# Optimization experiments

Hardware: AMD Instinct MI355X
Metric: run time of the kernel (lower is better)

Reference implementation:

```python
import jax, jax.numpy as jnp
import numpy as np
from jax import lax

N = 200; E = 3200; HID = 64; NH = 16; OUT = 2 * HID; CAT = NH * OUT  # CAT = 2048
ALPHA = 0.2


def _gat(h, e_attr, adj, n2n, W, a_s, a_d, a_e, We, concat):
    # edge-feature-aware GAT head: logits from Wh_i, Wh_j and projected node2node feats
    Nn = h.shape[0]
    Wh = h @ W                                       # [N, out]
    ee = ((n2n @ We) @ a_e).reshape(Nn, Nn)          # [N, N] edge-feature term
    logits = jax.nn.leaky_relu((Wh @ a_s)[:, None] + (Wh @ a_d)[None, :] + ee,
                               negative_slope=ALPHA)
    logits = jnp.where(adj > 0, logits, -1e9)        # mask to graph structure
    att = jax.nn.softmax(logits, axis=1)
    h2 = att @ Wh
    if concat:
        h2 = jax.nn.elu(h2)
    return h2, jax.nn.elu(e_attr @ We)               # updated node + edge features


def _edge_pool(x, eidx, e, w, b):
    # static-shape edge pooling: score edges, gate nodes by mean incident score
    src, dst = eidx[0], eidx[1]
    s = jax.nn.sigmoid(jnp.concatenate([x[src], x[dst], e], axis=1) @ w + b)  # [E]
    deg = jax.ops.segment_sum(jnp.ones_like(s), src, num_segments=x.shape[0])
    ns = jax.ops.segment_sum(s, src, num_segments=x.shape[0]) / (deg + 1e-6)
    return x * ns[:, None], e * s[:, None]


def _gpool(x, w, b):
    # GlobalAttention: gate_nn = Linear+Sigmoid, softmax over nodes, weighted sum
    gate = jax.nn.softmax(jax.nn.sigmoid(x @ w + b), axis=0)  # [N, 1]
    return jnp.sum(gate * x, axis=0, keepdims=True)           # [1, D]


def _adj_n2n(Nn, eidx, eattr):
    # vectorized version of the per-edge Python loop in _get_adj_node2node
    src, dst = eidx[0], eidx[1]
    adj = jnp.zeros((Nn, Nn), eattr.dtype).at[src, dst].set(1.0)
    n2n = jnp.zeros((Nn * Nn, eattr.shape[1]), eattr.dtype).at[src * Nn + dst].set(eattr)
    return adj, n2n


def _lstm_dir(x, Wih, Whh, b):
    # one LSTM direction over seq x [T, Din] (PyTorch i,f,g,o gate order)
    Hh = Whh.shape[1]
    def step(carry, xt):
        h, c = carry
        g = xt @ Wih.T + h @ Whh.T + b
        i, f, gg, o = jnp.split(g, 4)
        c = jax.nn.sigmoid(f) * c + jax.nn.sigmoid(i) * jnp.tanh(gg)
        h = jax.nn.sigmoid(o) * jnp.tanh(c)
        return (h, c), h
    (_, _), ys = lax.scan(step, (jnp.zeros(Hh, x.dtype), jnp.zeros(Hh, x.dtype)), x)
    return ys


def setup_inputs():
    key = jax.random.key(0)
    ks = iter(jax.random.split(key, 64))
    def rn(shape, scale=0.05):
        return jax.random.normal(next(ks), shape, jnp.float32) * scale
    inp = {}
    for g in (1, 2):
        eidx = jax.random.randint(next(ks), (2, E), 0, N)
        eattr = rn((E, HID), 1.0)
        adj, n2n = _adj_n2n(N, eidx, eattr)
        inp['features%d' % g] = rn((N, HID), 1.0)
        inp['edge_index%d' % g] = eidx
        inp['edgesAttr%d' % g] = eattr
        inp['adjacency%d' % g] = adj
        inp['node2node%d' % g] = n2n
    inp.update(dict(
        W_h=rn((HID, HID)),
        W_gat=rn((NH, HID, OUT)), a_src=rn((NH, OUT)), a_dst=rn((NH, OUT)),
        a_e=rn((NH, OUT)), We_gat=rn((NH, HID, OUT)),
        W_out=rn((CAT, OUT)), ao_src=rn((OUT,)), ao_dst=rn((OUT,)), ao_e=rn((OUT,)),
        We_out=rn((CAT, OUT)),
        ep1_w=rn((3 * CAT,)), ep1_b=rn(()),
        ep2_w=rn((3 * OUT,)), ep2_b=rn(()),
        g1_w=rn((HID, 1)), g1_b=rn((1,)),
        g2_w=rn((CAT, 1)), g2_b=rn((1,)),
        g3_w=rn((OUT, 1)), g3_b=rn((1,)),
        Wih0=rn((2, 512, 35 * HID)), Whh0=rn((2, 512, 128)), b0=rn((2, 512)),
        Wih1=rn((2, 512, 256)), Whh1=rn((2, 512, 128)), b1=rn((2, 512)),
        fc_w=rn((256, 2)), fc_b=rn((2,)),
    ))
    return inp


def reference(features1, features2, edge_index1, edge_index2, edgesAttr1, edgesAttr2,
              adjacency1, adjacency2, node2node1, node2node2,
              W_h, W_gat, a_src, a_dst, a_e, We_gat,
              W_out, ao_src, ao_dst, ao_e, We_out,
              ep1_w, ep1_b, ep2_w, ep2_b,
              g1_w, g1_b, g2_w, g2_b, g3_w, g3_b,
              Wih0, Whh0, b0, Wih1, Whh1, b1, fc_w, fc_b):
    def graph(feat, eidx, eattr, adj, n2n):
        h = jax.nn.elu(feat @ W_h)                              # SingleNodeAttentionLayer
        hs = [_gpool(h, g1_w, g1_b)]
        outs = [_gat(h, eattr, adj, n2n, W_gat[i], a_src[i], a_dst[i], a_e[i],
                     We_gat[i], True) for i in range(NH)]
        h = jnp.concatenate([o[0] for o in outs], axis=1)       # [N, 2048]
        eattr = jnp.concatenate([o[1] for o in outs], axis=1)   # [E, 2048]
        h, eattr = _edge_pool(h, eidx, eattr, ep1_w, ep1_b)
        hs.append(_gpool(h, g2_w, g2_b))
        adj2, n2n2 = _adj_n2n(h.shape[0], eidx, eattr)          # dense [N*N, 2048]
        h, eattr = _gat(h, eattr, adj2, n2n2, W_out, ao_src, ao_dst, ao_e, We_out, False)
        h, eattr = _edge_pool(h, eidx, eattr, ep2_w, ep2_b)
        hs.append(_gpool(h, g3_w, g3_b))
        return jnp.concatenate(hs, axis=1)                      # [1, 35*HID]

    h1 = graph(features1, edge_index1, edgesAttr1, adjacency1, node2node1)
    h2 = graph(features2, edge_index2, edgesAttr2, adjacency2, node2node2)
    x = jnp.concatenate([h1, h2], axis=0)                       # seq [2, 2240]
    for Wih, Whh, b in ((Wih0, Whh0, b0), (Wih1, Whh1, b1)):
        f = _lstm_dir(x, Wih[0], Whh[0], b[0])
        r = _lstm_dir(x[::-1], Wih[1], Whh[1], b[1])[::-1]
        x = jnp.concatenate([f, r], axis=1)                     # [2, 256]
    logits = x[-1] @ fc_w + fc_b
    return jax.nn.softmax(logits)[None, :]                      # [1, nclass]
```

## Files before the change

### kernel.cpp

```cpp
#include <hip/hip_runtime.h>
#include <math.h>

#define DI static __device__ __forceinline__

DI float eluf(float x){ return x > 0.f ? x : expm1f(x); }
DI float lreluf(float x){ return x > 0.f ? x : 0.2f*x; }
DI float sigmf(float x){ return 1.f/(1.f+expf(-x)); }

typedef unsigned short u16;
typedef unsigned int   u32;
typedef __attribute__((ext_vector_type(8))) short short8_t;
typedef __attribute__((ext_vector_type(4))) float f32x4;

DI u16 bf16rne(float f){
  u32 u = __float_as_uint(f);
  u += 0x7fffu + ((u>>16)&1u);
  return (u16)(u>>16);
}

DI f32x4 bmfma(short8_t a, short8_t b, f32x4 c){
  return __builtin_amdgcn_mfma_f32_16x16x32_bf16(a, b, c, 0, 0, 0);
}

constexpr int N=200, E=3200, HID=64, NH=16, OUTD=128, CAT=2048, SEQD=2240;

constexpr int OH0   = 0;
constexpr int OWH   = OH0 + N*HID;
constexpr int OASN  = OWH + NH*N*OUTD;
constexpr int OADN  = OASN + NH*N;
constexpr int OH1   = OADN + NH*N;
constexpr int OXW1  = OH1 + N*CAT;
constexpr int OXW2  = OXW1 + 256;
constexpr int OEW1  = OXW2 + 256;
constexpr int OS1   = OEW1 + E;
constexpr int ODEG1 = OS1 + E;
constexpr int OSS1  = ODEG1 + 256;
constexpr int ORAW1 = OSS1 + 256;
constexpr int OWH2  = ORAW1 + 256;
constexpr int OAS2  = OWH2 + N*OUTD;
constexpr int OAD2  = OAS2 + 256;
constexpr int OEWV  = OAD2 + 256;
constexpr int OH2B  = OEWV + E;
constexpr int OXS2  = OH2B + N*OUTD;
constexpr int OXD2  = OXS2 + 256;
constexpr int ODEG2 = OXD2 + 256;
constexpr int OSS2  = ODEG2 + 256;
constexpr int ORAW2 = OSS2 + 256;
constexpr int ORAW3 = ORAW2 + 256;
constexpr int PGF   = ORAW3 + 256;
constexpr int GLOBF = 10624;
constexpr int TOTF  = GLOBF + 2*PGF;

__device__ __attribute__((aligned(16))) float G_F[TOTF];
__device__ float G_E2PART[(size_t)4*2*E*OUTD];
__device__ float G_EDOTH[2*NH*E];
__device__ float G_WHHT[2*2*128*512];
__device__ int   G_PIDX[2*N*N];
__device__ __attribute__((aligned(16))) u16 G_WGAT_T[NH*OUTD*HID];
__device__ __attribute__((aligned(16))) u16 G_WOUT_T[OUTD*CAT];
__device__ __attribute__((aligned(16))) u16 G_EATTR_BF[2*E*HID];

DI float* gf(int g){ return G_F + GLOBF + (size_t)g*PGF; }
DI float* gwe_ae(){ return G_F; }
DI float* gv_e(){ return G_F + 1024; }
DI float* gy0(){ return G_F + 3072; }
DI float* gy1(){ return G_F + 3584; }
DI float* gxseq(){ return G_F + 4096; }
DI float* gxg(){ return G_F + 8576; }
DI int*   gpidx(int g){ return G_PIDX + g*N*N; }

struct GraphIn {
  const float *feat, *eattr, *adj, *n2n;
  const int   *eidx;
};

struct Params {
  GraphIn g[2];
  const float *W_h, *W_gat, *a_src, *a_dst, *a_e, *We_gat;
  const float *W_out, *ao_src, *ao_dst, *ao_e, *We_out;
  const float *ep1_w, *ep1_b, *ep2_w, *ep2_b;
  const float *g1_w, *g1_b, *g2_w, *g2_b, *g3_w, *g3_b;
  const float *Wih0, *Whh0, *b0, *Wih1, *Whh1, *b1, *fc_w, *fc_b;
  float *out;
};

constexpr int ZPG  = 2*E + 1024 + 768;
constexpr int IB_Z = (2*ZPG+255)/256;
constexpr int IB_C = (2*N*N+255)/256;
constexpr int IB_D = (2*2*512*128)/256;
constexpr int IB_E = (NH*HID+CAT+3)/4;
constexpr int IB_H = (2*N+3)/4;
constexpr int IB_W1 = (NH*OUTD*HID)/256;
constexpr int IB_W2 = (OUTD*CAT)/256;
constexpr int IB_EA = (2*E*HID)/256;
__global__ void k_init(Params P){
  int b = blockIdx.x, tid = threadIdx.x;
  if (b < IB_Z){
    int i = b*256 + tid;
    if (i < 2*ZPG){
      int g = i/ZPG, r = i%ZPG;
      int addr;
      if (r < E) addr = OEW1+r;
      else if (r < 2*E) addr = OEWV+(r-E);
      else if (r < 2*E+512) addr = ODEG1+(r-2*E);
      else if (r < 2*E+1024) addr = ODEG2+(r-2*E-512);
      else if (r < 2*E+1280) addr = OXW1+(r-2*E-1024);
      else if (r < 2*E+1536) addr = OXW2+(r-2*E-1280);
      else addr = ORAW2+(r-2*E-1536);
      gf(g)[addr] = 0.f;
    }
  } else if (b < IB_Z+IB_C){
    int i = (b-IB_Z)*256 + tid; if (i < 2*N*N) G_PIDX[i] = -1;
  } else if (b < IB_Z+IB_C+IB_D){
    int idx = (b-IB_Z-IB_C)*256 + tid;
    int l = idx >> 17;
    int r = idx & 131071;
    int d = r >> 16;
    int r2 = r & 65535;
    int gate = r2 & 511;
    int k = r2 >> 9;
    const float* Whh = l ? P.Whh1 : P.Whh0;
    G_WHHT[idx] = Whh[((size_t)d*512+gate)*128 + k];
  } else if (b < IB_Z+IB_C+IB_D+IB_E){
    int gid = (b-IB_Z-IB_C-IB_D)*4 + (tid>>6);
    int lane = tid & 63;
    if (gid < NH*HID){
      int h = gid/HID, c = gid%HID;
      const float* W = P.We_gat + (size_t)(h*HID+c)*OUTD;
      const float* a = P.a_e + h*OUTD;
      float acc = 0.f;
      for (int o=lane;o<OUTD;o+=64) acc += W[o]*a[o];
      for (int off=32;off>0;off>>=1) acc += __shfl_down(acc,off);
      if (lane==0) gwe_ae()[gid] = acc;
    } else if (gid < NH*HID+CAT){
      int c = gid - NH*HID;
      const float* W = P.We_out + (size_t)c*OUTD;
      float acc = 0.f;
      for (int o=lane;o<OUTD;o+=64) acc += W[o]*P.ao_e[o];
      for (int off=32;off>0;off>>=1) acc += __shfl_down(acc,off);
      if (lane==0) gv_e()[c] = acc;
    }
  } else if (b < IB_Z+IB_C+IB_D+IB_E+IB_H){
    int unit = (b-IB_Z-IB_C-IB_D-IB_E)*4 + (tid>>6);
    if (unit >= 2*N) return;
    int g = unit / N, n = unit % N, c = tid & 63;
    const float* feat = P.g[g].feat;
    float acc = 0.f;
    for (int k=0;k<HID;k++) acc += feat[n*HID+k]*P.W_h[k*HID+c];
    float v = eluf(acc);
    float* f = gf(g);
    f[OH0 + n*HID + c] = v;
    float r = v*P.g1_w[c];
    for (int off=32;off>0;off>>=1) r += __shfl_down(r,off);
    if (c==0) f[ORAW1+n] = r;
  } else if (b < IB_Z+IB_C+IB_D+IB_E+IB_H+IB_W1){
    int i = (b-(IB_Z+IB_C+IB_D+IB_E+IB_H))*256 + tid;
    int h = i>>13, o = (i>>6)&127, c = i&63;
    G_WGAT_T[i] = bf16rne(P.We_gat[(size_t)(h*HID+c)*OUTD + o]);
  } else if (b < IB_Z+IB_C+IB_D+IB_E+IB_H+IB_W1+IB_W2){
    int i = (b-(IB_Z+IB_C+IB_D+IB_E+IB_H+IB_W1))*256 + tid;
    int n = i>>11, q = i&2047;
    G_WOUT_T[i] = bf16rne(P.We_out[(size_t)q*OUTD + n]);
  } else {
    int i = (b-(IB_Z+IB_C+IB_D+IB_E+IB_H+IB_W1+IB_W2))*256 + tid;
    int g = i >= E*HID ? 1 : 0;
    G_EATTR_BF[i] = bf16rne(P.g[g].eattr[i - g*E*HID]);
  }
}
constexpr int IB_TOT = IB_Z+IB_C+IB_D+IB_E+IB_H+IB_W1+IB_W2+IB_EA;


DI void e2p_body(Params& P, int idx, char* smem){
  int g = idx/400, r2 = idx%400, hg = r2/100, eb = r2%100;
  int tid = threadIdx.x;
  int wave = tid>>6, lane = tid&63, l16 = lane&15, l4 = lane>>4;
  u16* Tlds = (u16*)smem;
  int e0 = eb*32;
  int nt0 = wave*2;
  const u16* ea = G_EATTR_BF + ((size_t)g*E + e0)*HID;
  short8_t af00 = *(const short8_t*)(ea + l16*HID + l4*8);
  short8_t af01 = *(const short8_t*)(ea + l16*HID + 32 + l4*8);
  short8_t af10 = *(const short8_t*)(ea + (16+l16)*HID + l4*8);
  short8_t af11 = *(const short8_t*)(ea + (16+l16)*HID + 32 + l4*8);
  float ew1p0[4] = {0.f,0.f,0.f,0.f}, ewvp0[4] = {0.f,0.f,0.f,0.f};
  float ew1p1[4] = {0.f,0.f,0.f,0.f}, ewvp1[4] = {0.f,0.f,0.f,0.f};
  for (int hh=0; hh<4; hh++){
    int h = hg*4 + hh;
    const u16* Wg = G_WGAT_T + (size_t)h*OUTD*HID;
    #pragma unroll
    for (int nn=0; nn<2; nn++){
      int nt = nt0 + nn;
      const u16* Wgn = Wg + (size_t)(nt*16 + l16)*HID + l4*8;
      short8_t wg0 = *(const short8_t*)Wgn;
      short8_t wg1 = *(const short8_t*)(Wgn + 32);
      f32x4 d0 = {0.f,0.f,0.f,0.f}, d1 = {0.f,0.f,0.f,0.f};
      d0 = bmfma(af00, wg0, d0);
      d1 = bmfma(af10, wg0, d1);
      d0 = bmfma(af01, wg1, d0);
      d1 = bmfma(af11, wg1, d1);
      int qg = h*OUTD + nt*16 + l16;
      float w1 = P.ep1_w[2*CAT + qg];
      float wv = gv_e()[qg];
      int qloc = hh*128 + nt*16 + l16;
      #pragma unroll
      for (int r=0;r<4;r++){
        float v0 = d0[r] > 0.f ? d0[r] : expm1f(d0[r]);
        float v1 = d1[r] > 0.f ? d1[r] : expm1f(d1[r]);
        ew1p0[r] += v0*w1; ewvp0[r] += v0*wv;
        ew1p1[r] += v1*w1; ewvp1[r] += v1*wv;
        int row = l4*4 + r;
        int byt = (row*1024 + qloc*2) ^ ((row&7)<<4);
        *(u16*)((char*)Tlds + byt) = bf16rne(v0);
        *(u16*)((char*)Tlds + byt + 16384) = bf16rne(v1);
      }
    }
  }
  const u16* WoA = G_WOUT_T + (size_t)(wave*32 + l16)*CAT + hg*512 + l4*8;
  const u16* WoB = WoA + 16*CAT;
  short8_t w0a = *(const short8_t*)WoA;
  short8_t w0b = *(const short8_t*)WoB;
  short8_t w1a = *(const short8_t*)(WoA + 32);
  short8_t w1b = *(const short8_t*)(WoB + 32);
  float* f = gf(g);
  #pragma unroll
  for (int r=0;r<4;r++){
    float a0 = ew1p0[r], b0 = ewvp0[r], a1 = ew1p1[r], b1 = ewvp1[r];
    a0 += __shfl_xor(a0,1); b0 += __shfl_xor(b0,1); a1 += __shfl_xor(a1,1); b1 += __shfl_xor(b1,1);
    a0 += __shfl_xor(a0,2); b0 += __shfl_xor(b0,2); a1 += __shfl_xor(a1,2); b1 += __shfl_xor(b1,2);
    a0 += __shfl_xor(a0,4); b0 += __shfl_xor(b0,4); a1 += __shfl_xor(a1,4); b1 += __shfl_xor(b1,4);
    a0 += __shfl_xor(a0,8); b0 += __shfl_xor(b0,8); a1 += __shfl_xor(a1,8); b1 += __shfl_xor(b1,8);
    if (l16==0){
      int e = e0 + l4*4 + r;
      atomicAdd(&f[OEW1+e], a0);
      atomicAdd(&f[OEWV+e], b0);
      atomicAdd(&f[OEW1+e+16], a1);
      atomicAdd(&f[OEWV+e+16], b1);
    }
  }
  __syncthreads();
  f32x4 acc00 = {0.f,0.f,0.f,0.f}, acc01 = {0.f,0.f,0.f,0.f};
  f32x4 acc10 = {0.f,0.f,0.f,0.f}, acc11 = {0.f,0.f,0.f,0.f};
  #pragma unroll
  for (int ks=0; ks<16; ks++){
    short8_t na = w0a, nb = w0b;
    if (ks < 14){
      na = *(const short8_t*)(WoA + (ks+2)*32);
      nb = *(const short8_t*)(WoB + (ks+2)*32);
    }
    int byt = (l16*1024 + ks*64 + l4*16) ^ ((l16&7)<<4);
    short8_t a0 = *(const short8_t*)((const char*)Tlds + byt);
    short8_t a1 = *(const short8_t*)((const char*)Tlds + byt + 16384);
    acc00 = bmfma(a0, w0a, acc00);
    acc10 = bmfma(a1, w0a, acc10);
    acc01 = bmfma(a0, w0b, acc01);
    acc11 = bmfma(a1, w0b, acc11);
    w0a = w1a; w0b = w1b; w1a = na; w1b = nb;
  }
  float* dst = G_E2PART + (((size_t)hg*2 + g)*E + e0)*OUTD;
  #pragma unroll
  for (int r=0;r<4;r++){
    int ee = l4*4 + r;
    dst[(size_t)ee*OUTD + wave*32 + l16]      = acc00[r];
    dst[(size_t)ee*OUTD + wave*32 + 16 + l16] = acc01[r];
    dst[(size_t)(16+ee)*OUTD + wave*32 + l16]      = acc10[r];
    dst[(size_t)(16+ee)*OUTD + wave*32 + 16 + l16] = acc11[r];
  }
}

DI void edoth_body(Params& P, int idx, float* s){
  int tid = threadIdx.x;
  int g = idx / (E/16);
  int e0 = (idx % (E/16)) * 16;
  float (*ea)[HID+1] = (float(*)[HID+1])s;
  float (*wa)[HID+1] = (float(*)[HID+1])(s + 16*(HID+1));
  {
    int row = tid >> 4, c0 = (tid & 15)*4;
    float4 v = *(const float4*)&P.g[g].eattr[(size_t)(e0+row)*HID + c0];
    ea[row][c0]=v.x; ea[row][c0+1]=v.y; ea[row][c0+2]=v.z; ea[row][c0+3]=v.w;
    float4 w = *(const float4*)&gwe_ae()[row*HID + c0];
    wa[row][c0]=w.x; wa[row][c0+1]=w.y; wa[row][c0+2]=w.z; wa[row][c0+3]=w.w;
  }
  __syncthreads();
  int h = tid >> 4, el = tid & 15;
  float acc = 0.f;
  #pragma unroll
  for (int c=0;c<HID;c++) acc += ea[el][c]*wa[h][c];
  G_EDOTH[((size_t)g*NH + h)*E + e0 + el] = acc;
}

DI void wh_body(Params& P, int idx, float* s){
  int o = threadIdx.x;
  if (o >= 128) return;
  int g = idx / (N*(NH+1));
  int r = idx % (N*(NH+1));
  int h = r / N, n = r % N;
  float* f = gf(g);
  if (h == NH){
    if (n != 0) return;
    float* att = s;
    float* sb  = s + 200;
    for (int j = o; j < N; j += 128) att[j] = sigmf(f[ORAW1+j] + P.g1_b[0]);
    __syncthreads();
    float m = -3e38f;
    for (int j = o; j < N; j += 128) m = fmaxf(m, att[j]);
    sb[o] = m; __syncthreads();
    for (int sft=64;sft>0;sft>>=1){ if (o<sft) sb[o]=fmaxf(sb[o],sb[o+sft]); __syncthreads(); }
    m = sb[0]; __syncthreads();
    float ss = 0.f;
    for (int j = o; j < N; j += 128){ float e = expf(att[j]-m); ss += e; }
    sb[o] = ss; __syncthreads();
    for (int sft=64;sft>0;sft>>=1){ if (o<sft) sb[o]+=sb[o+sft]; __syncthreads(); }
    float inv = 1.f/sb[0]; __syncthreads();
    for (int j = o; j < N; j += 128) att[j] = expf(att[j]-m)*inv;
    __syncthreads();
    if (o < HID){
      float acc = 0.f;
      for (int j=0;j<N;j++) acc += att[j]*f[OH0 + j*HID + o];
      gxseq()[g*SEQD + o] = acc;
    }
    return;
  }
  float* hs   = s;
  float* sred = s + 64;
  float* dred = s + 192;
  if (o < HID) hs[o] = f[OH0 + n*HID + o];
  __syncthreads();
  const float* W = P.W_gat + (size_t)h*HID*OUTD + o;
  float acc = 0.f;
  for (int c=0;c<HID;c++) acc += hs[c]*W[(size_t)c*OUTD];
  f[OWH + ((size_t)h*N + n)*OUTD + o] = acc;
  sred[o] = acc*P.a_src[h*OUTD+o];
  dred[o] = acc*P.a_dst[h*OUTD+o];
  __syncthreads();
  for (int sft=64;sft>0;sft>>=1){ if (o<sft){ sred[o]+=sred[o+sft]; dred[o]+=dred[o+sft]; } __syncthreads(); }
  if (o==0){ f[OASN+h*N+n]=sred[0]; f[OADN+h*N+n]=dred[0]; }
}

DI void pairs_body(Params& P, int idx){
  int g = idx / 13;
  int e = (idx % 13)*256 + threadIdx.x;
  if (e >= E) return;
  const int* ei = P.g[g].eidx;
  atomicMax(&gpidx(g)[ei[e]*N + ei[E+e]], e);
}

constexpr int MB_E2P = 800, MB_ED = 400, MB_WH = 2*N*(NH+1), MB_PR = 26;
__global__ __launch_bounds__(256) void k_mega(Params P){
  __shared__ __attribute__((aligned(16))) char smem[32768];
  int b = blockIdx.x;
  if (b < MB_E2P) e2p_body(P, b, smem);
  else if (b < MB_E2P+MB_ED) edoth_body(P, b-MB_E2P, (float*)smem);
  else if (b < MB_E2P+MB_ED+MB_WH) wh_body(P, b-(MB_E2P+MB_ED), (float*)smem);
  else pairs_body(P, b-(MB_E2P+MB_ED+MB_WH));
}

__global__ void k_att1(Params P){
  int nb = blockIdx.x, h = blockIdx.y, g = blockIdx.z, tid = threadIdx.x;
  int n0 = nb*4;
  __shared__ float z[4][N];
  __shared__ float red[128];
  __shared__ float sinv[4];
  __shared__ float lxr[2][12];
  float* f = gf(g);
  const float* adj = P.g[g].adj;
  const int* pidx = gpidx(g);
  const float* edoth = G_EDOTH + ((size_t)g*NH + h)*E;
  const float* adn = f + OADN + h*N;
  for (int i=0;i<4;i++){
    float asn = f[OASN + h*N + n0+i];
    for (int j = tid; j < N; j += 128){
      float a = adj[(n0+i)*N + j];
      float zz;
      if (a > 0.f){
        int p = pidx[(n0+i)*N + j];
        float ee = (p >= 0) ? edoth[p] : 0.f;
        zz = lreluf(asn + adn[j] + ee);
      } else zz = -1e9f;
      z[i][j] = zz;
    }
  }
  __syncthreads();
  for (int i=0;i<4;i++){
    float m = -3e38f;
    for (int j = tid; j < N; j += 128) m = fmaxf(m, z[i][j]);
    red[tid] = m; __syncthreads();
    for (int s=64;s>0;s>>=1){ if (tid<s) red[tid]=fmaxf(red[tid],red[tid+s]); __syncthreads(); }
    m = red[0]; __syncthreads();
    float ssum = 0.f;
    for (int j = tid; j < N; j += 128){ float e = expf(z[i][j]-m); z[i][j]=e; ssum += e; }
    red[tid] = ssum; __syncthreads();
    for (int s=64;s>0;s>>=1){ if (tid<s) red[tid]+=red[tid+s]; __syncthreads(); }
    if (tid==0) sinv[i] = 1.f/red[0];
    __syncthreads();
  }
  const float* wh = f + OWH + (size_t)h*N*OUTD;
  float a0=0.f,a1=0.f,a2=0.f,a3=0.f;
  for (int j=0;j<N;j++){
    float w = wh[(size_t)j*OUTD + tid];
    a0 += z[0][j]*w; a1 += z[1][j]*w; a2 += z[2][j]*w; a3 += z[3][j]*w;
  }
  float v0 = eluf(a0*sinv[0]);
  float v1 = eluf(a1*sinv[1]);
  float v2 = eluf(a2*sinv[2]);
  float v3 = eluf(a3*sinv[3]);
  f[OH1 + (size_t)(n0+0)*CAT + h*OUTD + tid] = v0;
  f[OH1 + (size_t)(n0+1)*CAT + h*OUTD + tid] = v1;
  f[OH1 + (size_t)(n0+2)*CAT + h*OUTD + tid] = v2;
  f[OH1 + (size_t)(n0+3)*CAT + h*OUTD + tid] = v3;
  float w1 = P.ep1_w[h*OUTD + tid];
  float w2 = P.ep1_w[CAT + h*OUTD + tid];
  float w3 = P.g2_w[h*OUTD + tid];
  float pp[12];
  pp[0]=v0*w1; pp[1]=v0*w2; pp[2]=v0*w3;
  pp[3]=v1*w1; pp[4]=v1*w2; pp[5]=v1*w3;
  pp[6]=v2*w1; pp[7]=v2*w2; pp[8]=v2*w3;
  pp[9]=v3*w1; pp[10]=v3*w2; pp[11]=v3*w3;
  #pragma unroll
  for (int k=0;k<12;k++){
    #pragma unroll
    for (int off=32;off>0;off>>=1) pp[k] += __shfl_down(pp[k],off);
  }
  int wv = tid>>6, ln = tid&63;
  if (ln==0){
    #pragma unroll
    for (int k=0;k<12;k++) lxr[wv][k]=pp[k];
  }
  __syncthreads();
  if (tid<12){
    float s = lxr[0][tid]+lxr[1][tid];
    int node = n0 + tid/3, kind = tid%3;
    int base = kind==0 ? OXW1 : (kind==1 ? OXW2 : ORAW2);
    atomicAdd(&f[base + node], s);
  }
}

DI void wh2_body(Params& P, int nq, int g, char* smem){
  float* hrow = (float*)smem;
  float* part = (float*)(smem + 32768);
  float* lred = (float*)(smem + 32768 + 8192);
  int tid = threadIdx.x;
  float* f = gf(g);
  int n0 = nq*4;
  for (int idx=tid; idx<4*CAT; idx+=512)
    hrow[idx] = f[OH1 + (size_t)(n0 + (idx>>11))*CAT + (idx&2047)];
  __syncthreads();
  int o = tid&127, kq = tid>>7;
  float acc0=0.f, acc1=0.f, acc2=0.f, acc3=0.f;
  const float* W = P.W_out + (size_t)(kq*512)*OUTD + o;
  const float* hA = hrow + kq*512;
  const float* hB = hA + CAT;
  const float* hC = hB + CAT;
  const float* hD = hC + CAT;
  for (int j=0;j<512;j++){
    float w = W[(size_t)j*OUTD];
    acc0 += hA[j]*w; acc1 += hB[j]*w; acc2 += hC[j]*w; acc3 += hD[j]*w;
  }
  part[(kq*4+0)*128+o]=acc0;
  part[(kq*4+1)*128+o]=acc1;
  part[(kq*4+2)*128+o]=acc2;
  part[(kq*4+3)*128+o]=acc3;
  __syncthreads();
  float a[4];
  #pragma unroll
  for (int i=0;i<4;i++)
    a[i] = part[(0*4+i)*128+o]+part[(1*4+i)*128+o]+part[(2*4+i)*128+o]+part[(3*4+i)*128+o];
  if (kq==0){
    #pragma unroll
    for (int i=0;i<4;i++) f[OWH2 + (size_t)(n0+i)*OUTD + o] = a[i];
  }
  float pr[8];
  #pragma unroll
  for (int i=0;i<4;i++){ pr[i*2] = a[i]*P.ao_src[o]; pr[i*2+1] = a[i]*P.ao_dst[o]; }
  #pragma unroll
  for (int k=0;k<8;k++){
    #pragma unroll
    for (int off=32;off>0;off>>=1) pr[k] += __shfl_down(pr[k],off);
  }
  int wv = tid>>6, ln = tid&63;
  if (wv<2 && ln==0){
    #pragma unroll
    for (int k=0;k<8;k++) lred[wv*8+k]=pr[k];
  }
  __syncthreads();
  if (tid<8){
    float s = lred[tid]+lred[8+tid];
    int node = n0 + (tid>>1);
    if (tid&1) f[OAD2+node]=s; else f[OAS2+node]=s;
  }
}

DI void s1_body(Params& P, int idx){
  int g = idx/7;
  int e = (idx%7)*512 + threadIdx.x;
  if (e >= E) return;
  float* f = gf(g);
  const int* ei = P.g[g].eidx;
  int s = ei[e], d = ei[E+e];
  float v = sigmf(f[OXW1+s] + f[OXW2+d] + f[OEW1+e] + P.ep1_b[0]);
  f[OS1+e] = v;
  atomicAdd(&f[OSS1+s], v);
  atomicAdd(&f[ODEG1+s], 1.f);
}

__global__ __launch_bounds__(512) void k_s1wh2(Params P){
  __shared__ __attribute__((aligned(16))) char smem[32768 + 8192 + 64];
  int b = blockIdx.x;
  if (b < 100) wh2_body(P, b>>1, b&1, smem);
  else s1_body(P, b-100);
}

DI void gpool_body(Params& P, int xoff, int D, int odeg, int rawoff,
                   const float* bb, int outoff, int cb, int g,
                   float* att, float* sb){
  int tid = threadIdx.x;
  float* f = gf(g);
  if (tid < N){
    float sc = f[odeg+256+tid]/(f[odeg+tid]+1e-6f);
    att[tid] = sigmf(f[rawoff+tid]*sc + bb[0]);
  }
  __syncthreads();
  float m = (tid < N) ? att[tid] : -3e38f;
  sb[tid] = m; __syncthreads();
  for (int s=256;s>0;s>>=1){ if (tid<s) sb[tid]=fmaxf(sb[tid],sb[tid+s]); __syncthreads(); }
  m = sb[0]; __syncthreads();
  float e = (tid < N) ? expf(att[tid]-m) : 0.f;
  sb[tid] = e; __syncthreads();
  for (int s=256;s>0;s>>=1){ if (tid<s) sb[tid]+=sb[tid+s]; __syncthreads(); }
  float inv = 1.f/sb[0]; __syncthreads();
  if (tid < N){
    float sc = f[odeg+256+tid]/(f[odeg+tid]+1e-6f);
    att[tid] = e*inv*sc;
  }
  __syncthreads();
  int c = cb*512 + tid;
  if (c < D){
    const float* x = f + xoff;
    float acc = 0.f;
    for (int n=0;n<N;n++) acc += att[n]*x[(size_t)n*D + c];
    gxseq()[g*SEQD + outoff + c] = acc;
  }
}

DI void att2_body(Params& P, int nb, int g, char* smem){
  int tid = threadIdx.x;
  int grp = tid>>7, o = tid&127;
  int n0 = nb*4, n = n0 + grp;
  float (*z)[N] = (float(*)[N])smem;
  float* nsv = (float*)(smem + 4*N*4);
  float* red = nsv + 256;
  float* inv = red + 512;
  float* lxr = inv + 4;
  float* f = gf(g);
  const float* adj = P.g[g].adj;
  const int* pidx = gpidx(g);
  for (int j = tid; j < N; j += 512)
    nsv[j] = f[OSS1+j]/(f[ODEG1+j]+1e-6f);
  __syncthreads();
  float asn = f[OAS2+n]*nsv[n];
  for (int j = o; j < N; j += 128){
    float a = adj[n*N + j];
    float zz;
    if (a > 0.f){
      int p = pidx[n*N + j];
      float ee = (p >= 0) ? f[OEWV+p]*f[OS1+p] : 0.f;
      zz = lreluf(asn + f[OAD2+j]*nsv[j] + ee);
    } else zz = -1e9f;
    z[grp][j] = zz;
  }
  __syncthreads();
  float m = -3e38f;
  for (int j = o; j < N; j += 128) m = fmaxf(m, z[grp][j]);
  red[grp*128+o] = m; __syncthreads();
  for (int s=64;s>0;s>>=1){ if (o<s) red[grp*128+o]=fmaxf(red[grp*128+o],red[grp*128+o+s]); __syncthreads(); }
  m = red[grp*128]; __syncthreads();
  float ssum = 0.f;
  for (int j = o; j < N; j += 128){ float e = expf(z[grp][j]-m); z[grp][j]=e; ssum += e; }
  red[grp*128+o] = ssum; __syncthreads();
  for (int s=64;s>0;s>>=1){ if (o<s) red[grp*128+o]+=red[grp*128+o+s]; __syncthreads(); }
  if (o==0) inv[grp] = 1.f/red[grp*128];
  __syncthreads();
  const float* wh = f + OWH2;
  float acc = 0.f;
  for (int j=0;j<N;j++){
    float w = z[grp][j]*nsv[j];
    if (w != 0.f) acc += w * wh[(size_t)j*OUTD + o];
  }
  float v = acc*inv[grp];
  f[OH2B + (size_t)n*OUTD + o] = v;
  float pr[3];
  pr[0] = v*P.ep2_w[o];
  pr[1] = v*P.ep2_w[OUTD+o];
  pr[2] = v*P.g3_w[o];
  #pragma unroll
  for (int k=0;k<3;k++){
    #pragma unroll
    for (int off=32;off>0;off>>=1) pr[k] += __shfl_down(pr[k],off);
  }
  int wv = tid>>6, ln = tid&63;
  if (ln==0){
    lxr[wv*3+0]=pr[0]; lxr[wv*3+1]=pr[1]; lxr[wv*3+2]=pr[2];
  }
  __syncthreads();
  if (tid<12){
    int node = tid/3, kind = tid%3;
    float s = lxr[(node*2)*3+kind] + lxr[(node*2+1)*3+kind];
    int base = kind==0 ? OXS2 : (kind==1 ? OXD2 : ORAW3);
    f[base + n0 + node] = s;
  }
}

__global__ __launch_bounds__(512) void k_att2p(Params P){
  __shared__ __attribute__((aligned(16))) char smem[8192];
  int b = blockIdx.x;
  if (b < 100) att2_body(P, b>>1, b&1, smem);
  else {
    int idx = b-100, g = idx>>2, cb = idx&3;
    float* att = (float*)smem;
    float* sb  = att + 256;
    gpool_body(P, OH1, CAT, ODEG1, ORAW2, P.g2_b, HID, cb, g, att, sb);
  }
}

constexpr int TE2 = 16;
__global__ void k_ew2fin(Params P){
  int e0 = blockIdx.x*TE2, g = blockIdx.y, tid = threadIdx.x;
  __shared__ float lred[2][TE2];
  float* f = gf(g);
  float w2 = P.ep2_w[2*OUTD + tid];
  int lane = tid & 63, wvi = tid >> 6;
  for (int e=0;e<TE2;e++){
    const float* src = G_E2PART + ((size_t)g*E + e0 + e)*OUTD + tid;
    float a = 0.f;
    #pragma unroll
    for (int h=0;h<4;h++) a += src[(size_t)h*2*E*OUTD];
    float v = eluf(f[OS1+e0+e]*a) * w2;
    for (int off=32;off>0;off>>=1) v += __shfl_down(v,off);
    if (lane==0) lred[wvi][e]=v;
  }
  __syncthreads();
  if (tid < TE2){
    int e = e0 + tid;
    float ew2 = lred[0][tid]+lred[1][tid];
    const int* ei = P.g[g].eidx;
    int s = ei[e], d = ei[E+e];
    float v = sigmf(f[OXS2+s] + f[OXD2+d] + ew2 + P.ep2_b[0]);
    atomicAdd(&f[OSS2+s], v);
    atomicAdd(&f[ODEG2+s], 1.f);
  }
}

__global__ __launch_bounds__(512) void k_pool3(Params P){
  __shared__ float att[256];
  __shared__ float sb[512];
  int g = blockIdx.x;
  gpool_body(P, OH2B, OUTD, ODEG2, ORAW3, P.g3_b, HID+CAT, 0, g, att, sb);
}

__global__ void k_lstm_xg(Params P, int layer){
  int gid = blockIdx.x*4 + (threadIdx.x>>6);
  int lane = threadIdx.x & 63;
  int t = gid >> 10;
  int rem = gid & 1023;
  int d = rem >> 9;
  int gate = rem & 511;
  const float* Wih = layer ? P.Wih1 : P.Wih0;
  const float* bb  = layer ? P.b1   : P.b0;
  const float* xin = layer ? gy0()  : gxseq();
  int Din = layer ? 256 : SEQD;
  const float* x = xin + t*Din;
  const float* Wr = Wih + ((size_t)d*512 + gate)*Din;
  float acc = 0.f;
  for (int k=lane; k<Din; k+=64) acc += x[k]*Wr[k];
  for (int off=32; off>0; off>>=1) acc += __shfl_down(acc, off);
  if (lane==0) gxg()[(t*2 + d)*512 + gate] = acc + bb[d*512 + gate];
}

__global__ void k_lstm_rec(Params P, int layer){
  int d = blockIdx.x, tid = threadIdx.x;
  float* yout = layer ? gy1() : gy0();
  const float* T = G_WHHT + (size_t)(layer*2 + d)*128*512;
  __shared__ float h[128], c[128], gbuf[512];
  if (tid < 128){ h[tid]=0.f; c[tid]=0.f; }
  __syncthreads();
  for (int s=0;s<2;s++){
    int t = (d==0) ? s : 1-s;
    float acc = gxg()[(t*2 + d)*512 + tid];
    for (int k=0;k<128;k++) acc += h[k]*T[(size_t)k*512 + tid];
    gbuf[tid] = acc;
    __syncthreads();
    if (tid < 128){
      float ii = sigmf(gbuf[tid]);
      float ff = sigmf(gbuf[128+tid]);
      float gg = tanhf(gbuf[256+tid]);
      float oo = sigmf(gbuf[384+tid]);
      float cn = ff*c[tid] + ii*gg;
      c[tid] = cn;
      float hn = oo*tanhf(cn);
      h[tid] = hn;
      yout[t*256 + d*128 + tid] = hn;
    }
    __syncthreads();
  }
}

__global__ __launch_bounds__(1024) void k_recfin(Params P){
  int tid = threadIdx.x;
  int d = tid>>9, gt = tid&511;
  __shared__ float h[2][128], c[2][128], gbuf[2][512], yfin[256];
  __shared__ float sb[256], sb2[256];
  if (gt < 128){ h[d][gt]=0.f; c[d][gt]=0.f; }
  __syncthreads();
  const float* T = G_WHHT + (size_t)(2 + d)*128*512;
  for (int s=0;s<2;s++){
    int t = (d==0) ? s : 1-s;
    float acc = gxg()[(t*2 + d)*512 + gt];
    for (int k=0;k<128;k++) acc += h[d][k]*T[(size_t)k*512 + gt];
    gbuf[d][gt] = acc;
    __syncthreads();
    if (gt < 128){
      float ii = sigmf(gbuf[d][gt]);
      float ff = sigmf(gbuf[d][128+gt]);
      float gg = tanhf(gbuf[d][256+gt]);
      float oo = sigmf(gbuf[d][384+gt]);
      float cn = ff*c[d][gt] + ii*gg;
      c[d][gt] = cn;
      float hn = oo*tanhf(cn);
      h[d][gt] = hn;
      if (t==1) yfin[d*128 + gt] = hn;
    }
    __syncthreads();
  }
  if (tid < 256){
    sb[tid]  = yfin[tid]*P.fc_w[tid*2+0];
    sb2[tid] = yfin[tid]*P.fc_w[tid*2+1];
  }
  __syncthreads();
  for (int s=128;s>0;s>>=1){
    if (tid<s){ sb[tid]+=sb[tid+s]; sb2[tid]+=sb2[tid+s]; }
    __syncthreads();
  }
  if (tid==0){
    float l0 = sb[0] + P.fc_b[0];
    float l1 = sb2[0] + P.fc_b[1];
    float m = fmaxf(l0,l1);
    float e0 = expf(l0-m), e1 = expf(l1-m), inv = 1.f/(e0+e1);
    P.out[0] = e0*inv;
    P.out[1] = e1*inv;
  }
}

extern "C" void kernel_launch(void* const* d_in, const int* in_sizes, int n_in,
                              void* d_out, int out_size, void* d_ws, size_t ws_size,
                              hipStream_t stream){
  Params P;
  for (int g=0; g<2; ++g){
    int b = g*5;
    P.g[g].feat  = (const float*)d_in[b+0];
    P.g[g].eidx  = (const int*)d_in[b+1];
    P.g[g].eattr = (const float*)d_in[b+2];
    P.g[g].adj   = (const float*)d_in[b+3];
    P.g[g].n2n   = (const float*)d_in[b+4];
  }
  P.W_h   = (const float*)d_in[10];
  P.W_gat = (const float*)d_in[11];
  P.a_src = (const float*)d_in[12];
  P.a_dst = (const float*)d_in[13];
  P.a_e   = (const float*)d_in[14];
  P.We_gat= (const float*)d_in[15];
  P.W_out = (const float*)d_in[16];
  P.ao_src= (const float*)d_in[17];
  P.ao_dst= (const float*)d_in[18];
  P.ao_e  = (const float*)d_in[19];
  P.We_out= (const float*)d_in[20];
  P.ep1_w = (const float*)d_in[21];
  P.ep1_b = (const float*)d_in[22];
  P.ep2_w = (const float*)d_in[23];
  P.ep2_b = (const float*)d_in[24];
  P.g1_w  = (const float*)d_in[25];
  P.g1_b  = (const float*)d_in[26];
  P.g2_w  = (const float*)d_in[27];
  P.g2_b  = (const float*)d_in[28];
  P.g3_w  = (const float*)d_in[29];
  P.g3_b  = (const float*)d_in[30];
  P.Wih0  = (const float*)d_in[31];
  P.Whh0  = (const float*)d_in[32];
  P.b0    = (const float*)d_in[33];
  P.Wih1  = (const float*)d_in[34];
  P.Whh1  = (const float*)d_in[35];
  P.b1    = (const float*)d_in[36];
  P.fc_w  = (const float*)d_in[37];
  P.fc_b  = (const float*)d_in[38];
  P.out   = (float*)d_out;

  k_init <<<dim3(IB_TOT), 256, 0, stream>>>(P);
  k_mega <<<dim3(MB_E2P+MB_ED+MB_WH+MB_PR), 256, 0, stream>>>(P);
  k_att1 <<<dim3(N/4,NH,2),128, 0, stream>>>(P);
  k_s1wh2<<<dim3(114),    512, 0, stream>>>(P);
  k_att2p<<<dim3(108),    512, 0, stream>>>(P);
  k_ew2fin<<<dim3(E/TE2,2),128, 0, stream>>>(P);
  k_pool3<<<dim3(2),      512, 0, stream>>>(P);
  k_lstm_xg <<<dim3(512), 256, 0, stream>>>(P, 0);
  k_lstm_rec<<<dim3(2),   512, 0, stream>>>(P, 0);
  k_lstm_xg <<<dim3(512), 256, 0, stream>>>(P, 1);
  k_recfin<<<dim3(1),    1024, 0, stream>>>(P);
}
```

Measured before the change: 345.5 us.

## Fuse edge-pool finish with LSTM input projection and pool3 into recurrence

The init kernel now transposes Whh, We_gat and We_out through padded shared-memory tiles with coalesced reads and writes, in far fewer blocks. The standalone bf16 copy of edge attributes is dropped, and the MFMA kernel converts fp32 edge attributes to bf16 at load time. The layer-0 LSTM input projection over the first 2112 features runs concurrently with the edge-pool finish in one launch. The final global pool and the projection of the last 128 features are folded into the layer-0 recurrence kernel. Together this removes several launches and serial tail work, in exchange for redundant pooling in both direction blocks and more complex kernels.

```diff
diff --git a/kernel.cpp b/kernel.cpp
--- a/kernel.cpp
+++ b/kernel.cpp
@@ -20,6 +20,15 @@
 
 DI f32x4 bmfma(short8_t a, short8_t b, f32x4 c){
   return __builtin_amdgcn_mfma_f32_16x16x32_bf16(a, b, c, 0, 0, 0);
+}
+
+DI short8_t cvt8(const float* p){
+  float4 a = *(const float4*)p;
+  float4 bq = *(const float4*)(p+4);
+  short8_t r;
+  r[0]=(short)bf16rne(a.x); r[1]=(short)bf16rne(a.y); r[2]=(short)bf16rne(a.z); r[3]=(short)bf16rne(a.w);
+  r[4]=(short)bf16rne(bq.x); r[5]=(short)bf16rne(bq.y); r[6]=(short)bf16rne(bq.z); r[7]=(short)bf16rne(bq.w);
+  return r;
 }
 
 constexpr int N=200, E=3200, HID=64, NH=16, OUTD=128, CAT=2048, SEQD=2240;
@@ -58,7 +67,6 @@
 __device__ int   G_PIDX[2*N*N];
 __device__ __attribute__((aligned(16))) u16 G_WGAT_T[NH*OUTD*HID];
 __device__ __attribute__((aligned(16))) u16 G_WOUT_T[OUTD*CAT];
-__device__ __attribute__((aligned(16))) u16 G_EATTR_BF[2*E*HID];
 
 DI float* gf(int g){ return G_F + GLOBF + (size_t)g*PGF; }
 DI float* gwe_ae(){ return G_F; }
@@ -87,13 +95,14 @@
 constexpr int ZPG  = 2*E + 1024 + 768;
 constexpr int IB_Z = (2*ZPG+255)/256;
 constexpr int IB_C = (2*N*N+255)/256;
-constexpr int IB_D = (2*2*512*128)/256;
+constexpr int IB_D = 32;
 constexpr int IB_E = (NH*HID+CAT+3)/4;
 constexpr int IB_H = (2*N+3)/4;
-constexpr int IB_W1 = (NH*OUTD*HID)/256;
-constexpr int IB_W2 = (OUTD*CAT)/256;
-constexpr int IB_EA = (2*E*HID)/256;
-__global__ void k_init(Params P){
+constexpr int IB_W1 = 16;
+constexpr int IB_W2 = 32;
+constexpr int IB_TOT = IB_Z+IB_C+IB_D+IB_E+IB_H+IB_W1+IB_W2;
+__global__ __launch_bounds__(256) void k_init(Params P){
+  __shared__ __attribute__((aligned(16))) float ldt[8320];
   int b = blockIdx.x, tid = threadIdx.x;
   if (b < IB_Z){
     int i = b*256 + tid;
@@ -112,15 +121,25 @@
   } else if (b < IB_Z+IB_C){
     int i = (b-IB_Z)*256 + tid; if (i < 2*N*N) G_PIDX[i] = -1;
   } else if (b < IB_Z+IB_C+IB_D){
-    int idx = (b-IB_Z-IB_C)*256 + tid;
-    int l = idx >> 17;
-    int r = idx & 131071;
-    int d = r >> 16;
-    int r2 = r & 65535;
-    int gate = r2 & 511;
-    int k = r2 >> 9;
+    int tt = b-(IB_Z+IB_C);
+    int ld = tt>>3, gt0 = (tt&7)*64;
+    int l = ld>>1, d = ld&1;
     const float* Whh = l ? P.Whh1 : P.Whh0;
-    G_WHHT[idx] = Whh[((size_t)d*512+gate)*128 + k];
+    const float* src = Whh + ((size_t)d*512 + gt0)*128;
+    #pragma unroll
+    for (int i=0;i<32;i++){
+      int idx = tid + i*256;
+      int gl = idx>>7, k = idx&127;
+      ldt[gl*129 + k] = src[idx];
+    }
+    __syncthreads();
+    float* dst = G_WHHT + (size_t)ld*128*512 + gt0;
+    #pragma unroll
+    for (int i=0;i<32;i++){
+      int idx = tid + i*256;
+      int gl = idx&63, k = idx>>6;
+      dst[(size_t)k*512 + gl] = ldt[gl*129 + k];
+    }
   } else if (b < IB_Z+IB_C+IB_D+IB_E){
     int gid = (b-IB_Z-IB_C-IB_D)*4 + (tid>>6);
     int lane = tid & 63;
@@ -154,20 +173,40 @@
     for (int off=32;off>0;off>>=1) r += __shfl_down(r,off);
     if (c==0) f[ORAW1+n] = r;
   } else if (b < IB_Z+IB_C+IB_D+IB_E+IB_H+IB_W1){
-    int i = (b-(IB_Z+IB_C+IB_D+IB_E+IB_H))*256 + tid;
-    int h = i>>13, o = (i>>6)&127, c = i&63;
-    G_WGAT_T[i] = bf16rne(P.We_gat[(size_t)(h*HID+c)*OUTD + o]);
-  } else if (b < IB_Z+IB_C+IB_D+IB_E+IB_H+IB_W1+IB_W2){
-    int i = (b-(IB_Z+IB_C+IB_D+IB_E+IB_H+IB_W1))*256 + tid;
-    int n = i>>11, q = i&2047;
-    G_WOUT_T[i] = bf16rne(P.We_out[(size_t)q*OUTD + n]);
+    int h = b-(IB_Z+IB_C+IB_D+IB_E+IB_H);
+    const float* src = P.We_gat + (size_t)h*HID*OUTD;
+    #pragma unroll
+    for (int i=0;i<32;i++){
+      int idx = tid + i*256;
+      int c = idx>>7, o = idx&127;
+      ldt[o*65 + c] = src[idx];
+    }
+    __syncthreads();
+    u16* dst = G_WGAT_T + (size_t)h*OUTD*HID;
+    #pragma unroll
+    for (int i=0;i<32;i++){
+      int idx = tid + i*256;
+      int c = idx&63, o = idx>>6;
+      dst[o*64 + c] = bf16rne(ldt[o*65 + c]);
+    }
   } else {
-    int i = (b-(IB_Z+IB_C+IB_D+IB_E+IB_H+IB_W1+IB_W2))*256 + tid;
-    int g = i >= E*HID ? 1 : 0;
-    G_EATTR_BF[i] = bf16rne(P.g[g].eattr[i - g*E*HID]);
-  }
-}
-constexpr int IB_TOT = IB_Z+IB_C+IB_D+IB_E+IB_H+IB_W1+IB_W2+IB_EA;
+    int tt = b-(IB_Z+IB_C+IB_D+IB_E+IB_H+IB_W1);
+    int q0 = (tt>>1)*128, n0 = (tt&1)*64;
+    #pragma unroll
+    for (int i=0;i<32;i++){
+      int idx = tid + i*256;
+      int nl = idx&63, ql = idx>>6;
+      ldt[ql*65 + nl] = P.We_out[(size_t)(q0+ql)*OUTD + n0 + nl];
+    }
+    __syncthreads();
+    #pragma unroll
+    for (int i=0;i<32;i++){
+      int idx = tid + i*256;
+      int ql = idx&127, nl = idx>>7;
+      G_WOUT_T[(size_t)(n0+nl)*CAT + q0 + ql] = bf16rne(ldt[ql*65 + nl]);
+    }
+  }
+}
 
 
 DI void e2p_body(Params& P, int idx, char* smem){
@@ -177,11 +216,11 @@
   u16* Tlds = (u16*)smem;
   int e0 = eb*32;
   int nt0 = wave*2;
-  const u16* ea = G_EATTR_BF + ((size_t)g*E + e0)*HID;
-  short8_t af00 = *(const short8_t*)(ea + l16*HID + l4*8);
-  short8_t af01 = *(const short8_t*)(ea + l16*HID + 32 + l4*8);
-  short8_t af10 = *(const short8_t*)(ea + (16+l16)*HID + l4*8);
-  short8_t af11 = *(const short8_t*)(ea + (16+l16)*HID + 32 + l4*8);
+  const float* eaf = P.g[g].eattr + (size_t)e0*HID;
+  short8_t af00 = cvt8(eaf + l16*HID + l4*8);
+  short8_t af01 = cvt8(eaf + l16*HID + 32 + l4*8);
+  short8_t af10 = cvt8(eaf + (16+l16)*HID + l4*8);
+  short8_t af11 = cvt8(eaf + (16+l16)*HID + 32 + l4*8);
   float ew1p0[4] = {0.f,0.f,0.f,0.f}, ewvp0[4] = {0.f,0.f,0.f,0.f};
   float ew1p1[4] = {0.f,0.f,0.f,0.f}, ewvp1[4] = {0.f,0.f,0.f,0.f};
   for (int hh=0; hh<4; hh++){
@@ -622,8 +661,8 @@
 }
 
 constexpr int TE2 = 16;
-__global__ void k_ew2fin(Params P){
-  int e0 = blockIdx.x*TE2, g = blockIdx.y, tid = threadIdx.x;
+DI void ew2fin_body(Params& P, int eb, int g){
+  int e0 = eb*TE2, tid = threadIdx.x;
   __shared__ float lred[2][TE2];
   float* f = gf(g);
   float w2 = P.ep2_w[2*OUTD + tid];
@@ -649,11 +688,81 @@
   }
 }
 
-__global__ __launch_bounds__(512) void k_pool3(Params P){
-  __shared__ float att[256];
-  __shared__ float sb[512];
-  int g = blockIdx.x;
-  gpool_body(P, OH2B, OUTD, ODEG2, ORAW3, P.g3_b, HID+CAT, 0, g, att, sb);
+DI void xga_body(Params& P, int idx){
+  int gid = idx*2 + (threadIdx.x>>6);
+  int lane = threadIdx.x & 63;
+  int t = gid >> 10, rem = gid & 1023, d = rem>>9, gate = rem&511;
+  const float* x = gxseq() + t*SEQD;
+  const float* Wr = P.Wih0 + ((size_t)d*512 + gate)*SEQD;
+  float acc = 0.f;
+  for (int k=lane; k<2112; k+=64) acc += x[k]*Wr[k];
+  for (int off=32; off>0; off>>=1) acc += __shfl_down(acc, off);
+  if (lane==0) gxg()[(t*2 + d)*512 + gate] = acc + P.b0[d*512 + gate];
+}
+
+__global__ __launch_bounds__(128) void k_ew2xg(Params P){
+  int b = blockIdx.x;
+  if (b < 400) ew2fin_body(P, b%200, b/200);
+  else xga_body(P, b-400);
+}
+
+__global__ __launch_bounds__(512) void k_rec0(Params P){
+  int d = blockIdx.x, tid = threadIdx.x;
+  __shared__ float xtail[2][128];
+  __shared__ float att[256], sb[512];
+  for (int g=0; g<2; ++g){
+    float* f = gf(g);
+    if (tid < N){
+      float sc = f[ODEG2+256+tid]/(f[ODEG2+tid]+1e-6f);
+      att[tid] = sigmf(f[ORAW3+tid]*sc + P.g3_b[0]);
+    }
+    __syncthreads();
+    float m = (tid < N) ? att[tid] : -3e38f;
+    sb[tid] = m; __syncthreads();
+    for (int s=256;s>0;s>>=1){ if (tid<s) sb[tid]=fmaxf(sb[tid],sb[tid+s]); __syncthreads(); }
+    m = sb[0]; __syncthreads();
+    float e = (tid < N) ? expf(att[tid]-m) : 0.f;
+    sb[tid] = e; __syncthreads();
+    for (int s=256;s>0;s>>=1){ if (tid<s) sb[tid]+=sb[tid+s]; __syncthreads(); }
+    float inv = 1.f/sb[0]; __syncthreads();
+    if (tid < N){
+      float sc = f[ODEG2+256+tid]/(f[ODEG2+tid]+1e-6f);
+      att[tid] = e*inv*sc;
+    }
+    __syncthreads();
+    if (tid < 128){
+      float acc = 0.f;
+      for (int n=0;n<N;n++) acc += att[n]*f[OH2B + (size_t)n*OUTD + tid];
+      xtail[g][tid] = acc;
+    }
+    __syncthreads();
+  }
+  __shared__ float h[128], c[128], gbuf[512];
+  if (tid < 128){ h[tid]=0.f; c[tid]=0.f; }
+  __syncthreads();
+  const float* T = G_WHHT + (size_t)d*128*512;
+  for (int s=0;s<2;s++){
+    int t = (d==0) ? s : 1-s;
+    float acc = gxg()[(t*2 + d)*512 + tid];
+    const float* wr = P.Wih0 + ((size_t)d*512 + tid)*SEQD + 2112;
+    const float* xt = xtail[t];
+    for (int k=0;k<128;k++) acc += xt[k]*wr[k];
+    for (int k=0;k<128;k++) acc += h[k]*T[(size_t)k*512 + tid];
+    gbuf[tid] = acc;
+    __syncthreads();
+    if (tid < 128){
+      float ii = sigmf(gbuf[tid]);
+      float ff = sigmf(gbuf[128+tid]);
+      float gg = tanhf(gbuf[256+tid]);
+      float oo = sigmf(gbuf[384+tid]);
+      float cn = ff*c[tid] + ii*gg;
+      c[tid] = cn;
+      float hn = oo*tanhf(cn);
+      h[tid] = hn;
+      gy0()[t*256 + d*128 + tid] = hn;
+    }
+    __syncthreads();
+  }
 }
 
 __global__ void k_lstm_xg(Params P, int layer){
@@ -673,34 +782,6 @@
   for (int k=lane; k<Din; k+=64) acc += x[k]*Wr[k];
   for (int off=32; off>0; off>>=1) acc += __shfl_down(acc, off);
   if (lane==0) gxg()[(t*2 + d)*512 + gate] = acc + bb[d*512 + gate];
-}
-
-__global__ void k_lstm_rec(Params P, int layer){
-  int d = blockIdx.x, tid = threadIdx.x;
-  float* yout = layer ? gy1() : gy0();
-  const float* T = G_WHHT + (size_t)(layer*2 + d)*128*512;
-  __shared__ float h[128], c[128], gbuf[512];
-  if (tid < 128){ h[tid]=0.f; c[tid]=0.f; }
-  __syncthreads();
-  for (int s=0;s<2;s++){
-    int t = (d==0) ? s : 1-s;
-    float acc = gxg()[(t*2 + d)*512 + tid];
-    for (int k=0;k<128;k++) acc += h[k]*T[(size_t)k*512 + tid];
-    gbuf[tid] = acc;
-    __syncthreads();
-    if (tid < 128){
-      float ii = sigmf(gbuf[tid]);
-      float ff = sigmf(gbuf[128+tid]);
-      float gg = tanhf(gbuf[256+tid]);
-      float oo = sigmf(gbuf[384+tid]);
-      float cn = ff*c[tid] + ii*gg;
-      c[tid] = cn;
-      float hn = oo*tanhf(cn);
-      h[tid] = hn;
-      yout[t*256 + d*128 + tid] = hn;
-    }
-    __syncthreads();
-  }
 }
 
 __global__ __launch_bounds__(1024) void k_recfin(Params P){
@@ -797,10 +878,8 @@
   k_att1 <<<dim3(N/4,NH,2),128, 0, stream>>>(P);
   k_s1wh2<<<dim3(114),    512, 0, stream>>>(P);
   k_att2p<<<dim3(108),    512, 0, stream>>>(P);
-  k_ew2fin<<<dim3(E/TE2,2),128, 0, stream>>>(P);
-  k_pool3<<<dim3(2),      512, 0, stream>>>(P);
-  k_lstm_xg <<<dim3(512), 256, 0, stream>>>(P, 0);
-  k_lstm_rec<<<dim3(2),   512, 0, stream>>>(P, 0);
-  k_lstm_xg <<<dim3(512), 256, 0, stream>>>(P, 1);
+  k_ew2xg<<<dim3(1424),   128, 0, stream>>>(P);
+  k_rec0 <<<dim3(2),      512, 0, stream>>>(P);
+  k_lstm_xg<<<dim3(512),  256, 0, stream>>>(P, 1);
   k_recfin<<<dim3(1),    1024, 0, stream>>>(P);
 }
```

Result: slower. 364.0 us (+5.4%).
